# Optimization experiments

Measured on AMD Instinct MI355X. Metric: run time of the kernel, lower is better.

Reference implementation:

```python
import jax, jax.numpy as jnp
import numpy as np

KS = 3  # kernel_size
PAD = (KS - 1) // 2  # 'auto' padding preserves spatial dims for stride=1


def setup_inputs() -> dict:
    key = jax.random.key(0)
    kq, kk, kv = jax.random.split(key, 3)
    shape = (8, 64, 256, 256)  # (b, c, H, W)
    q = jax.random.normal(kq, shape, dtype=jnp.float32)
    k = jax.random.normal(kk, shape, dtype=jnp.float32)
    v = jax.random.normal(kv, shape, dtype=jnp.float32)
    return {"q": q, "k": k, "v": v}


def _conv_attention(q, k, v):
    # q, k, v: (b, c, H, W). Local 3x3 window attention:
    # score_j = <q_center, k_neighbor_j>_c ; w = softmax_j(score) ; out = sum_j w_j * v_neighbor_j
    b, c, H, W = q.shape
    pad = ((0, 0), (0, 0), (PAD, PAD), (PAD, PAD))
    kp = jnp.pad(k, pad)  # zeros padding_mode
    vp = jnp.pad(v, pad)
    # scores over the KS*KS neighbors: fixed small loop over offsets (no data-dim loop)
    scores = []
    for dy in range(KS):
        for dx in range(KS):
            k_sh = kp[:, :, dy:dy + H, dx:dx + W]  # (b, c, H, W)
            scores.append(jnp.einsum('bchw,bchw->bhw', q, k_sh))
    s = jnp.stack(scores, axis=-1)            # (b, H, W, K)
    w = jax.nn.softmax(s, axis=-1)            # softmax over neighborhood
    out = jnp.zeros_like(q)
    i = 0
    for dy in range(KS):
        for dx in range(KS):
            v_sh = vp[:, :, dy:dy + H, dx:dx + W]  # (b, c, H, W)
            out = out + w[..., i][:, None] * v_sh
            i += 1
    return out  # (b, c, H, W)


def reference(q, k, v):
    return _conv_attention(q, k, v)
```

## Files before the change

kernel.cpp:

```cpp
#include <hip/hip_runtime.h>


constexpr int B = 8, C = 64, H = 256, W = 256;

__global__ __launch_bounds__(256) void conv_attn_kernel(
    const float* __restrict__ qg, const float* __restrict__ kg,
    const float* __restrict__ vg, float* __restrict__ og) {
  const int lane = threadIdx.x & 63;
  const int wv   = threadIdx.x >> 6;
  const int y    = blockIdx.x * 4 + wv;
  const int b    = blockIdx.y;
  const size_t cs   = (size_t)H * W;
  const size_t base = ((size_t)b * C) * cs + (size_t)y * W + lane * 4;
  const bool up_ok = (y > 0), dn_ok = (y < H - 1);
  const float4 z4 = make_float4(0.f, 0.f, 0.f, 0.f);

  float s[4][9];
#pragma unroll
  for (int j = 0; j < 4; ++j)
#pragma unroll
    for (int t = 0; t < 9; ++t) s[j][t] = 0.f;

#pragma unroll 2
  for (int c = 0; c < C; ++c) {
    const float* qp = qg + base + c * cs;
    const float* kp = kg + base + c * cs;
    float4 qv = *(const float4*)qp;
    float qa[4] = {qv.x, qv.y, qv.z, qv.w};
    float4 kr[3];
    kr[0] = up_ok ? *(const float4*)(kp - W) : z4;
    kr[1] = *(const float4*)kp;
    kr[2] = dn_ok ? *(const float4*)(kp + W) : z4;
#pragma unroll
    for (int dy = 0; dy < 3; ++dy) {
      float lf = __shfl_up(kr[dy].w, 1u);
      if (lane == 0) lf = 0.f;
      float rt = __shfl_down(kr[dy].x, 1u);
      if (lane == 63) rt = 0.f;
      float col[6] = {lf, kr[dy].x, kr[dy].y, kr[dy].z, kr[dy].w, rt};
#pragma unroll
      for (int j = 0; j < 4; ++j)
#pragma unroll
        for (int dx = 0; dx < 3; ++dx)
          s[j][dy * 3 + dx] = fmaf(qa[j], col[j + dx], s[j][dy * 3 + dx]);
    }
  }

#pragma unroll
  for (int j = 0; j < 4; ++j) {
    float m = s[j][0];
#pragma unroll
    for (int t = 1; t < 9; ++t) m = fmaxf(m, s[j][t]);
    float sum = 0.f;
#pragma unroll
    for (int t = 0; t < 9; ++t) { s[j][t] = __expf(s[j][t] - m); sum += s[j][t]; }
    float inv = 1.f / sum;
#pragma unroll
    for (int t = 0; t < 9; ++t) s[j][t] *= inv;
  }

#pragma unroll 2
  for (int c = 0; c < C; ++c) {
    const float* vp = vg + base + c * cs;
    float4 vr[3];
    vr[0] = up_ok ? *(const float4*)(vp - W) : z4;
    vr[1] = *(const float4*)vp;
    vr[2] = dn_ok ? *(const float4*)(vp + W) : z4;
    float o[4] = {0.f, 0.f, 0.f, 0.f};
#pragma unroll
    for (int dy = 0; dy < 3; ++dy) {
      float lf = __shfl_up(vr[dy].w, 1u);
      if (lane == 0) lf = 0.f;
      float rt = __shfl_down(vr[dy].x, 1u);
      if (lane == 63) rt = 0.f;
      float col[6] = {lf, vr[dy].x, vr[dy].y, vr[dy].z, vr[dy].w, rt};
#pragma unroll
      for (int j = 0; j < 4; ++j)
#pragma unroll
        for (int dx = 0; dx < 3; ++dx)
          o[j] = fmaf(s[j][dy * 3 + dx], col[j + dx], o[j]);
    }
    *(float4*)(og + base + c * cs) = make_float4(o[0], o[1], o[2], o[3]);
  }
}

extern "C" void kernel_launch(void* const* d_in, const int* in_sizes, int n_in,
                              void* d_out, int out_size, void* d_ws, size_t ws_size,
                              hipStream_t stream) {
  const float* q = (const float*)d_in[0];
  const float* k = (const float*)d_in[1];
  const float* v = (const float*)d_in[2];
  float* out = (float*)d_out;
  dim3 grid(H / 4, B);
  conv_attn_kernel<<<grid, dim3(256), 0, stream>>>(q, k, v, out);
}
```

Before: 431.4 us.

## Map one pixel per thread with scalar neighbor loads and swizzled block order

Replaces the 4-pixels-per-lane float4 layout with one pixel per thread, so each block covers one full image row and the grid grows fourfold. Horizontal neighbors now come from scalar loads at offsets ±1 served by cache, replacing the cross-lane shuffles. Block indices are swizzled across batches and launch bounds request 8 blocks per CU to raise occupancy. In exchange, each thread issues nine scalar loads per channel instead of three float4 loads, and each q element feeds fewer FMAs.

```diff
diff --git a/kernel.cpp b/kernel.cpp
--- a/kernel.cpp
+++ b/kernel.cpp
@@ -3,84 +3,97 @@
 
 constexpr int B = 8, C = 64, H = 256, W = 256;
 
-__global__ __launch_bounds__(256) void conv_attn_kernel(
+__global__ __launch_bounds__(256, 8) void conv_attn_kernel(
     const float* __restrict__ qg, const float* __restrict__ kg,
     const float* __restrict__ vg, float* __restrict__ og) {
-  const int lane = threadIdx.x & 63;
-  const int wv   = threadIdx.x >> 6;
-  const int y    = blockIdx.x * 4 + wv;
-  const int b    = blockIdx.y;
+  const int lin = blockIdx.y * (int)gridDim.x + blockIdx.x;
+  const int swz = (lin & 7) * ((H * B) / 8) + (lin >> 3);
+  const int y = swz & (H - 1);
+  const int b = swz >> 8;
+  const int x = threadIdx.x;
+
   const size_t cs   = (size_t)H * W;
-  const size_t base = ((size_t)b * C) * cs + (size_t)y * W + lane * 4;
-  const bool up_ok = (y > 0), dn_ok = (y < H - 1);
-  const float4 z4 = make_float4(0.f, 0.f, 0.f, 0.f);
+  const size_t base = ((size_t)b * C) * cs + (size_t)y * W + x;
+  const bool up = (y > 0), dn = (y < H - 1);
+  const bool lok = (x > 0), rok = (x < W - 1);
 
-  float s[4][9];
+  float s[9];
 #pragma unroll
-  for (int j = 0; j < 4; ++j)
-#pragma unroll
-    for (int t = 0; t < 9; ++t) s[j][t] = 0.f;
+  for (int t = 0; t < 9; ++t) s[t] = 0.f;
 
 #pragma unroll 2
   for (int c = 0; c < C; ++c) {
-    const float* qp = qg + base + c * cs;
-    const float* kp = kg + base + c * cs;
-    float4 qv = *(const float4*)qp;
-    float qa[4] = {qv.x, qv.y, qv.z, qv.w};
-    float4 kr[3];
-    kr[0] = up_ok ? *(const float4*)(kp - W) : z4;
-    kr[1] = *(const float4*)kp;
-    kr[2] = dn_ok ? *(const float4*)(kp + W) : z4;
-#pragma unroll
-    for (int dy = 0; dy < 3; ++dy) {
-      float lf = __shfl_up(kr[dy].w, 1u);
-      if (lane == 0) lf = 0.f;
-      float rt = __shfl_down(kr[dy].x, 1u);
-      if (lane == 63) rt = 0.f;
-      float col[6] = {lf, kr[dy].x, kr[dy].y, kr[dy].z, kr[dy].w, rt};
-#pragma unroll
-      for (int j = 0; j < 4; ++j)
-#pragma unroll
-        for (int dx = 0; dx < 3; ++dx)
-          s[j][dy * 3 + dx] = fmaf(qa[j], col[j + dx], s[j][dy * 3 + dx]);
+    const size_t cb = base + (size_t)c * cs;
+    const float qv = qg[cb];
+    const float* kp = kg + cb;
+    {
+      float a = (up && lok) ? kp[-W - 1] : 0.f;
+      float m = up ? kp[-W] : 0.f;
+      float r = (up && rok) ? kp[-W + 1] : 0.f;
+      s[0] = fmaf(qv, a, s[0]);
+      s[1] = fmaf(qv, m, s[1]);
+      s[2] = fmaf(qv, r, s[2]);
+    }
+    {
+      float a = lok ? kp[-1] : 0.f;
+      float m = kp[0];
+      float r = rok ? kp[1] : 0.f;
+      s[3] = fmaf(qv, a, s[3]);
+      s[4] = fmaf(qv, m, s[4]);
+      s[5] = fmaf(qv, r, s[5]);
+    }
+    {
+      float a = (dn && lok) ? kp[W - 1] : 0.f;
+      float m = dn ? kp[W] : 0.f;
+      float r = (dn && rok) ? kp[W + 1] : 0.f;
+      s[6] = fmaf(qv, a, s[6]);
+      s[7] = fmaf(qv, m, s[7]);
+      s[8] = fmaf(qv, r, s[8]);
     }
   }
 
+  {
+    float m = s[0];
 #pragma unroll
-  for (int j = 0; j < 4; ++j) {
-    float m = s[j][0];
-#pragma unroll
-    for (int t = 1; t < 9; ++t) m = fmaxf(m, s[j][t]);
+    for (int t = 1; t < 9; ++t) m = fmaxf(m, s[t]);
     float sum = 0.f;
 #pragma unroll
-    for (int t = 0; t < 9; ++t) { s[j][t] = __expf(s[j][t] - m); sum += s[j][t]; }
+    for (int t = 0; t < 9; ++t) { s[t] = __expf(s[t] - m); sum += s[t]; }
     float inv = 1.f / sum;
 #pragma unroll
-    for (int t = 0; t < 9; ++t) s[j][t] *= inv;
+    for (int t = 0; t < 9; ++t) s[t] *= inv;
   }
 
 #pragma unroll 2
   for (int c = 0; c < C; ++c) {
-    const float* vp = vg + base + c * cs;
-    float4 vr[3];
-    vr[0] = up_ok ? *(const float4*)(vp - W) : z4;
-    vr[1] = *(const float4*)vp;
-    vr[2] = dn_ok ? *(const float4*)(vp + W) : z4;
-    float o[4] = {0.f, 0.f, 0.f, 0.f};
-#pragma unroll
-    for (int dy = 0; dy < 3; ++dy) {
-      float lf = __shfl_up(vr[dy].w, 1u);
-      if (lane == 0) lf = 0.f;
-      float rt = __shfl_down(vr[dy].x, 1u);
-      if (lane == 63) rt = 0.f;
-      float col[6] = {lf, vr[dy].x, vr[dy].y, vr[dy].z, vr[dy].w, rt};
-#pragma unroll
-      for (int j = 0; j < 4; ++j)
-#pragma unroll
-        for (int dx = 0; dx < 3; ++dx)
-          o[j] = fmaf(s[j][dy * 3 + dx], col[j + dx], o[j]);
+    const size_t cb = base + (size_t)c * cs;
+    const float* vp = vg + cb;
+    float o = 0.f;
+    {
+      float a = (up && lok) ? vp[-W - 1] : 0.f;
+      float m = up ? vp[-W] : 0.f;
+      float r = (up && rok) ? vp[-W + 1] : 0.f;
+      o = fmaf(s[0], a, o);
+      o = fmaf(s[1], m, o);
+      o = fmaf(s[2], r, o);
     }
-    *(float4*)(og + base + c * cs) = make_float4(o[0], o[1], o[2], o[3]);
+    {
+      float a = lok ? vp[-1] : 0.f;
+      float m = vp[0];
+      float r = rok ? vp[1] : 0.f;
+      o = fmaf(s[3], a, o);
+      o = fmaf(s[4], m, o);
+      o = fmaf(s[5], r, o);
+    }
+    {
+      float a = (dn && lok) ? vp[W - 1] : 0.f;
+      float m = dn ? vp[W] : 0.f;
+      float r = (dn && rok) ? vp[W + 1] : 0.f;
+      o = fmaf(s[6], a, o);
+      o = fmaf(s[7], m, o);
+      o = fmaf(s[8], r, o);
+    }
+    og[cb] = o;
   }
 }
 
@@ -91,6 +104,6 @@
   const float* k = (const float*)d_in[1];
   const float* v = (const float*)d_in[2];
   float* out = (float*)d_out;
-  dim3 grid(H / 4, B);
+  dim3 grid(H, B);
   conv_attn_kernel<<<grid, dim3(256), 0, stream>>>(q, k, v, out);
 }
```

Result: slower. 444.3 us (+3.0%).

## Split channel reduction across waves per row with LDS reduction and block swizzle

Applied to the files above, without the earlier changes.

Each block now handles one image row, and its four waves each cover a quarter of the channels instead of four separate rows. Partial scores are combined through shared memory before the softmax, and each wave then produces output for its own channel slice. A block-index swizzle spreads consecutive blocks across rows and batches, and launch bounds request higher occupancy. This raises the block count and shortens the serial channel loop per wave, at the cost of LDS traffic and barriers, and of each wave recomputing the same softmax.

```diff
diff --git a/kernel.cpp b/kernel.cpp
--- a/kernel.cpp
+++ b/kernel.cpp
@@ -2,16 +2,21 @@
 
 
 constexpr int B = 8, C = 64, H = 256, W = 256;
+constexpr int CPW = C / 4;
 
-__global__ __launch_bounds__(256) void conv_attn_kernel(
+__global__ __launch_bounds__(256, 8) void conv_attn_kernel(
     const float* __restrict__ qg, const float* __restrict__ kg,
     const float* __restrict__ vg, float* __restrict__ og) {
+  const int lin = blockIdx.y * (int)gridDim.x + blockIdx.x;
+  const int swz = (lin & 7) * ((H * B) / 8) + (lin >> 3);
+  const int y    = swz & (H - 1);
+  const int b    = swz >> 8;
   const int lane = threadIdx.x & 63;
   const int wv   = threadIdx.x >> 6;
-  const int y    = blockIdx.x * 4 + wv;
-  const int b    = blockIdx.y;
-  const size_t cs   = (size_t)H * W;
-  const size_t base = ((size_t)b * C) * cs + (size_t)y * W + lane * 4;
+  const int c0   = wv * CPW;
+
+  const size_t cs    = (size_t)H * W;
+  const size_t ibase = (size_t)b * C * cs + (size_t)y * W + lane * 4;
   const bool up_ok = (y > 0), dn_ok = (y < H - 1);
   const float4 z4 = make_float4(0.f, 0.f, 0.f, 0.f);
 
@@ -22,11 +27,11 @@
     for (int t = 0; t < 9; ++t) s[j][t] = 0.f;
 
 #pragma unroll 2
-  for (int c = 0; c < C; ++c) {
-    const float* qp = qg + base + c * cs;
-    const float* kp = kg + base + c * cs;
-    float4 qv = *(const float4*)qp;
+  for (int ci = 0; ci < CPW; ++ci) {
+    const size_t cb = ibase + (size_t)(c0 + ci) * cs;
+    float4 qv = *(const float4*)(qg + cb);
     float qa[4] = {qv.x, qv.y, qv.z, qv.w};
+    const float* kp = kg + cb;
     float4 kr[3];
     kr[0] = up_ok ? *(const float4*)(kp - W) : z4;
     kr[1] = *(const float4*)kp;
@@ -46,6 +51,24 @@
     }
   }
 
+  __shared__ float red[256][9];
+#pragma unroll
+  for (int j = 0; j < 4; ++j) {
+    if (j) __syncthreads();
+#pragma unroll
+    for (int t = 0; t < 9; ++t) red[threadIdx.x][t] = s[j][t];
+    __syncthreads();
+    float tot[9];
+#pragma unroll
+    for (int t = 0; t < 9; ++t) tot[t] = 0.f;
+#pragma unroll
+    for (int w2 = 0; w2 < 4; ++w2)
+#pragma unroll
+      for (int t = 0; t < 9; ++t) tot[t] += red[w2 * 64 + lane][t];
+#pragma unroll
+    for (int t = 0; t < 9; ++t) s[j][t] = tot[t];
+  }
+
 #pragma unroll
   for (int j = 0; j < 4; ++j) {
     float m = s[j][0];
@@ -60,8 +83,9 @@
   }
 
 #pragma unroll 2
-  for (int c = 0; c < C; ++c) {
-    const float* vp = vg + base + c * cs;
+  for (int ci = 0; ci < CPW; ++ci) {
+    const size_t cb = ibase + (size_t)(c0 + ci) * cs;
+    const float* vp = vg + cb;
     float4 vr[3];
     vr[0] = up_ok ? *(const float4*)(vp - W) : z4;
     vr[1] = *(const float4*)vp;
@@ -80,7 +104,7 @@
         for (int dx = 0; dx < 3; ++dx)
           o[j] = fmaf(s[j][dy * 3 + dx], col[j + dx], o[j]);
     }
-    *(float4*)(og + base + c * cs) = make_float4(o[0], o[1], o[2], o[3]);
+    *(float4*)(og + cb) = make_float4(o[0], o[1], o[2], o[3]);
   }
 }
 
@@ -91,6 +115,6 @@
   const float* k = (const float*)d_in[1];
   const float* v = (const float*)d_in[2];
   float* out = (float*)d_out;
-  dim3 grid(H / 4, B);
+  dim3 grid(H, B);
   conv_attn_kernel<<<grid, dim3(256), 0, stream>>>(q, k, v, out);
 }
```

Result: slower. 631.3 us (+46.4%).
